# Optimization experiments

Measured on AMD Instinct MI355X. Metric: run time of the kernel, lower is better.

## Reference

```python
import jax, jax.numpy as jnp
import numpy as np
from jax import lax

B, IC, OC, H, W_DIM, K = 8, 64, 64, 256, 512, 3
BLUR_1D = [1.0, 3.0, 3.0, 1.0]
FACTOR = 2
GAIN = 1.0


def _blur_kernel():
    # setup_resample_kernel: outer product of 1D kernel, normalized to sum 1
    k = np.asarray(BLUR_1D, dtype=np.float32)
    k = np.outer(k, k)
    k = k / np.sum(k)
    return k  # [4,4]


def setup_inputs() -> dict:
    key = jax.random.key(0)
    ks = jax.random.split(key, 5)
    x = jax.random.normal(ks[0], (B, IC, H, H), dtype=jnp.float32)
    w = jax.random.normal(ks[1], (B, W_DIM), dtype=jnp.float32)
    # init_std = 1.0 for both weights since lrmul = 1.0
    w_conv = jax.random.normal(ks[2], (K, K, IC, OC), dtype=jnp.float32)
    w_dense = jax.random.normal(ks[3], (W_DIM, IC), dtype=jnp.float32)
    b_mod = jnp.zeros((IC,), dtype=jnp.float32)
    return {"x": x, "w": w, "w_conv": w_conv, "w_dense": w_dense, "b_mod": b_mod}


def reference(x, w, w_conv, w_dense, b_mod):
    k = w_conv.shape[0]
    ic, oc = w_conv.shape[2], w_conv.shape[3]

    # runtime coefs (equalized lr): he_std = gain / sqrt(fan_in), lrmul = 1
    coef_conv = 1.0 / np.sqrt(k * k * ic)
    coef_dense = 1.0 / np.sqrt(w.shape[1])

    # style = Dense(w) + bias (linear act, gain 1) + 1.0   -> [B, IC]
    style = w @ (coef_dense * w_dense) + b_mod + 1.0

    # modulate: [B,k,k,IC,OC]
    wmod = (coef_conv * w_conv)[None] * style[:, None, None, :, None]
    # demodulate over (kh, kw, ic)
    d = lax.rsqrt(jnp.sum(jnp.square(wmod), axis=(1, 2, 3)) + 1e-8)  # [B,OC]
    wmod = wmod * d[:, None, None, None, :]

    # per-sample grouped transposed conv (upsample x2) == lhs-dilated cross-corr
    # with the unflipped modulated weight, padding k-1 on each side.
    w_oihw = jnp.transpose(wmod, (0, 4, 3, 1, 2))  # [B,OC,IC,k,k]

    def up_conv(xb, wb):
        return lax.conv_general_dilated(
            xb[None], wb, window_strides=(1, 1),
            padding=[(k - 1, k - 1), (k - 1, k - 1)],
            lhs_dilation=(FACTOR, FACTOR),
            dimension_numbers=("NCHW", "OIHW", "NCHW"))[0]

    y = jax.vmap(up_conv)(x, w_oihw)  # [B,OC,(H-1)*2+k,(W-1)*2+k] = [B,OC,513,513]

    # upfirdn blur: kernel scaled by gain * factor**2, pad0 = pad1 = 1,
    # true convolution (kernel flipped in reference) applied depthwise.
    kb = jnp.asarray(_blur_kernel() * (GAIN * FACTOR ** 2))  # [4,4]
    fw = kb[::-1, ::-1][None, None]  # [1,1,4,4]
    b_, c_, s1, s2 = y.shape
    y = lax.conv_general_dilated(
        y.reshape(b_ * c_, 1, s1, s2), fw, window_strides=(1, 1),
        padding=[(1, 1), (1, 1)],
        dimension_numbers=("NCHW", "OIHW", "NCHW"))
    # output spatial: s1 + 2 - 4 + 1 = 2H
    return y.reshape(b_, c_, y.shape[2], y.shape[3])
```

## Files before the change

kernel.cpp:

```cpp
#include <hip/hip_runtime.h>

#define NB 8
#define IC 64
#define OC 64
#define HH 256
#define WD 512

typedef __bf16 bf16x8 __attribute__((ext_vector_type(8)));
typedef float f32x16 __attribute__((ext_vector_type(16)));
typedef float f32x2 __attribute__((ext_vector_type(2)));

__global__ __launch_bounds__(64) void style_kernel(
    const float* __restrict__ w, const float* __restrict__ w_dense,
    const float* __restrict__ b_mod, float* __restrict__ style) {
  const int b = blockIdx.x;
  const int ic = threadIdx.x;
  const float coef_dense = 0.044194173824159216f;
  const float* wr = w + b * WD;
  float acc = 0.f;
  for (int k = 0; k < WD; ++k) acc = fmaf(wr[k], w_dense[k * IC + ic], acc);
  style[b * IC + ic] = acc * coef_dense + b_mod[ic] + 1.0f;
}

__device__ inline void compute_E(const float* __restrict__ w_conv,
                                 const float* __restrict__ style, int b, int oc,
                                 int ic, float E[6][6]) {
  const float coef_conv = 1.0f / 24.0f;
  const float s = style[b * IC + ic] * coef_conv;

  float wm[3][3];
  float ssq = 0.f;
  #pragma unroll
  for (int kh = 0; kh < 3; ++kh)
    #pragma unroll
    for (int kw = 0; kw < 3; ++kw) {
      float v = w_conv[((kh * 3 + kw) * IC + ic) * OC + oc] * s;
      wm[kh][kw] = v;
      ssq += v * v;
    }
  #pragma unroll
  for (int off = 32; off > 0; off >>= 1) ssq += __shfl_xor(ssq, off);
  const float d = rsqrtf(ssq + 1e-8f);
  #pragma unroll
  for (int kh = 0; kh < 3; ++kh)
    #pragma unroll
    for (int kw = 0; kw < 3; ++kw) wm[kh][kw] *= d;

  const float g[4] = {0.25f, 0.75f, 0.75f, 0.25f};
  #pragma unroll
  for (int a = 0; a < 6; ++a)
    #pragma unroll
    for (int c = 0; c < 6; ++c) {
      float acc = 0.f;
      #pragma unroll
      for (int dh = 0; dh < 3; ++dh) {
        int u = a - dh;
        if (u < 0 || u > 3) continue;
        #pragma unroll
        for (int dw = 0; dw < 3; ++dw) {
          int v = c - dw;
          if (v < 0 || v > 3) continue;
          acc = fmaf(wm[dh][dw], g[u] * g[v], acc);
        }
      }
      E[a][c] = acc;
    }
}

__global__ __launch_bounds__(64) void pwf_kernel(
    const float* __restrict__ w_conv, const float* __restrict__ style,
    __bf16* __restrict__ PWf) {
  const int oc = blockIdx.x;
  const int b = blockIdx.y;
  const int ic = threadIdx.x;

  float E[6][6];
  compute_E(w_conv, style, b, oc, ic, E);

  const int ks = ic >> 4;
  const int h = (ic >> 3) & 1;
  const int e = ic & 7;
  const int lane = (oc & 31) + 32 * h;
  const int ocg = oc >> 5;

  #pragma unroll
  for (int pp = 0; pp < 2; ++pp)
    #pragma unroll
    for (int pq = 0; pq < 2; ++pq) {
      const int ph = pp * 2 + pq;
      #pragma unroll
      for (int j = 0; j < 3; ++j)
        #pragma unroll
        for (int l = 0; l < 3; ++l) {
          const int tap = j * 3 + l;
          float val = E[2 * j + 1 - pp][2 * l + 1 - pq];
          size_t off =
              ((size_t)(((((b * 4 + ph) * 9 + tap) * 2 + ocg) * 4 + ks)) * 64 +
               lane) * 8 + e;
          PWf[off] = (__bf16)val;
        }
    }
}

__global__ __launch_bounds__(256) void xt_kernel(const float* __restrict__ x,
                                                 __bf16* __restrict__ xT) {
  __shared__ unsigned short buf[64 * 257];
  const int tid = threadIdx.x;
  const int m = blockIdx.x;
  const int b = blockIdx.y;

  for (int ic = 0; ic < 64; ++ic) {
    float v = x[((size_t)(b * 64 + ic) * 256 + m) * 256 + tid];
    __bf16 bv = (__bf16)v;
    buf[ic * 257 + tid] = __builtin_bit_cast(unsigned short, bv);
  }
  __syncthreads();
  bf16x8* xTv = (bf16x8*)xT;
  #pragma unroll
  for (int it = 0; it < 8; ++it) {
    int pix = it * 32 + (tid >> 3);
    int g = tid & 7;
    bf16x8 o;
    #pragma unroll
    for (int e = 0; e < 8; ++e) {
      unsigned short u = buf[(g * 8 + e) * 257 + pix];
      o[e] = __builtin_bit_cast(__bf16, u);
    }
    xTv[((size_t)(b * 256 + m) * 256 + pix) * 8 + g] = o;
  }
}

#define CMT 16
#define CNT 32
#define XR 18
#define XC 34

__device__ __forceinline__ void loadA(const bf16x8* __restrict__ Av, int phb,
                                      int ocg, int ks, int l, int lane,
                                      bf16x8 A[3][2]) {
  #pragma unroll
  for (int j = 0; j < 3; ++j) {
    const int tap = j * 3 + l;
    #pragma unroll
    for (int pq = 0; pq < 2; ++pq)
      A[j][pq] =
          Av[(size_t)((((phb + pq) * 9 + tap) * 2 + ocg) * 4 + ks) * 64 + lane];
  }
}

__global__ __launch_bounds__(512, 2) void conv32_kernel(
    const __bf16* __restrict__ xT, const __bf16* __restrict__ PWf,
    float* __restrict__ out) {
  __shared__ bf16x8 xs[XR * XC * 8];

  const int tid = threadIdx.x;
  const int lane = tid & 63;
  const int w = tid >> 6;
  const int pp = w & 1;
  const int rh = w >> 1;

  const int bx = blockIdx.x;
  const int mtile = bx >> 3;
  const int ntile = bx & 7;
  const int ocg = blockIdx.y;
  const int b = blockIdx.z;
  const int m0 = mtile * CMT;
  const int n0 = ntile * CNT;

  const bf16x8* xTv = (const bf16x8*)xT;
  #pragma unroll
  for (int itr = 0; itr < 10; ++itr) {
    int lin = itr * 512 + tid;
    if (lin < XR * XC * 8) {
      int g = lin & 7;
      int pix = lin >> 3;
      int col = pix % XC;
      int row = pix / XC;
      int gr = m0 - 1 + row;
      int gc = n0 - 1 + col;
      bf16x8 v;
      if ((unsigned)gr < 256u && (unsigned)gc < 256u) {
        v = xTv[((size_t)(b * 256 + gr) * 256 + gc) * 8 + g];
      } else {
        #pragma unroll
        for (int e = 0; e < 8; ++e) v[e] = (__bf16)0.f;
      }
      xs[pix * 8 + (g ^ (col & 7))] = v;
    }
  }
  __syncthreads();

  f32x16 acc[4][2];
  #pragma unroll
  for (int mw = 0; mw < 4; ++mw)
    #pragma unroll
    for (int pq = 0; pq < 2; ++pq)
      #pragma unroll
      for (int e = 0; e < 16; ++e) acc[mw][pq][e] = 0.f;

  const int ln31 = lane & 31;
  const int lh = lane >> 5;
  const bf16x8* Av = (const bf16x8*)PWf;
  const int phb = b * 4 + pp * 2;

  bf16x8 Ac[3][2], An[3][2];
  loadA(Av, phb, ocg, 0, 0, lane, Ac);

  int ks = 0, l = 0;
  #pragma unroll 1
  for (int it = 0; it < 12; ++it) {
    const int ln = (l == 2) ? 0 : l + 1;
    const int ksn = ((l == 2) ? ks + 1 : ks) & 3;
    loadA(Av, phb, ocg, ksn, ln, lane, An);

    bf16x8 Bf[6];
    const int col_t = ln31 + l;
    const int gneed = ks * 2 + lh;
    #pragma unroll
    for (int r = 0; r < 6; ++r) {
      const int lds_row = 4 * rh + r;
      Bf[r] = xs[(lds_row * XC + col_t) * 8 + (gneed ^ (col_t & 7))];
    }

    __builtin_amdgcn_s_setprio(1);
    #pragma unroll
    for (int r = 0; r < 6; ++r) {
      #pragma unroll
      for (int j = 0; j < 3; ++j) {
        const int mw = r - j;
        if (mw >= 0 && mw < 4) {
          acc[mw][0] = __builtin_amdgcn_mfma_f32_32x32x16_bf16(
              Ac[j][0], Bf[r], acc[mw][0], 0, 0, 0);
          acc[mw][1] = __builtin_amdgcn_mfma_f32_32x32x16_bf16(
              Ac[j][1], Bf[r], acc[mw][1], 0, 0, 0);
        }
      }
    }
    __builtin_amdgcn_s_setprio(0);

    #pragma unroll
    for (int j = 0; j < 3; ++j)
      #pragma unroll
      for (int pq = 0; pq < 2; ++pq) Ac[j][pq] = An[j][pq];
    ks = ksn;
    l = ln;
  }

  #pragma unroll
  for (int mw = 0; mw < 4; ++mw) {
    const int p = 2 * (m0 + 4 * rh + mw) + pp;
    #pragma unroll
    for (int rr = 0; rr < 16; ++rr) {
      const int oc_loc = (rr & 3) + 8 * (rr >> 2) + 4 * lh;
      const int oc = ocg * 32 + oc_loc;
      size_t off = ((size_t)(b * 64 + oc) * 512 + p) * 512 + 2 * n0 + 2 * ln31;
      f32x2 v2;
      v2[0] = acc[mw][0][rr];
      v2[1] = acc[mw][1][rr];
      *(f32x2*)(out + off) = v2;
    }
  }
}

__global__ __launch_bounds__(64) void pw_kernel(
    const float* __restrict__ w_conv, const float* __restrict__ style,
    float* __restrict__ PW) {
  const int oc = blockIdx.x;
  const int b = blockIdx.y;
  const int ic = threadIdx.x;
  float E[6][6];
  compute_E(w_conv, style, b, oc, ic, E);
  #pragma unroll
  for (int pp = 0; pp < 2; ++pp)
    #pragma unroll
    for (int pq = 0; pq < 2; ++pq)
      #pragma unroll
      for (int j = 0; j < 3; ++j)
        #pragma unroll
        for (int l = 0; l < 3; ++l)
          PW[(((size_t)((b * 4 + pp * 2 + pq) * OC + oc) * IC + ic) * 9) +
             j * 3 + l] = E[2 * j + 1 - pp][2 * l + 1 - pq];
}

#define MT 16
#define NT 64
#define ICC 8
#define XROWS 18
#define XCOLS 66
#define XSTRIDE 68

__global__ __launch_bounds__(256) void conv_kernel(
    const float* __restrict__ x, const float* __restrict__ PW,
    float* __restrict__ out) {
  __shared__ float lds_x[ICC][XROWS][XSTRIDE];
  __shared__ float lds_w[4][ICC][9][4];

  const int tid = threadIdx.x;
  const int tn = tid & 15;
  const int tm = tid >> 4;
  const int bx = blockIdx.x;
  const int ntile = bx & 3;
  const int mtile = bx >> 2;
  const int ocg = blockIdx.y;
  const int b = blockIdx.z;
  const int m0 = mtile * MT;
  const int n0 = ntile * NT;

  float acc[4][4][4];
  #pragma unroll
  for (int o = 0; o < 4; ++o)
    #pragma unroll
    for (int ph = 0; ph < 4; ++ph)
      #pragma unroll
      for (int s = 0; s < 4; ++s) acc[o][ph][s] = 0.f;

  for (int ic0 = 0; ic0 < IC; ic0 += ICC) {
    __syncthreads();
    for (int ici = 0; ici < ICC; ++ici) {
      const float* xsrc = x + (size_t)(b * IC + ic0 + ici) * HH * HH;
      for (int rc = tid; rc < XROWS * XCOLS; rc += 256) {
        int r = rc / XCOLS;
        int c = rc - r * XCOLS;
        int gr = m0 - 1 + r;
        int gc = n0 - 1 + c;
        float v = 0.f;
        if ((unsigned)gr < HH && (unsigned)gc < HH) v = xsrc[gr * HH + gc];
        lds_x[ici][r][c] = v;
      }
    }
    for (int idx = tid; idx < 4 * ICC * 9 * 4; idx += 256) {
      int o = idx / (ICC * 9 * 4);
      int rem = idx - o * (ICC * 9 * 4);
      int ici = rem / 36;
      int r2 = rem - ici * 36;
      int t = r2 >> 2;
      int ph = r2 & 3;
      lds_w[o][ici][t][ph] =
          PW[(((size_t)((b * 4 + ph) * OC + (ocg * 4 + o)) * IC +
               (ic0 + ici)) * 9) + t];
    }
    __syncthreads();
    for (int ici = 0; ici < ICC; ++ici) {
      #pragma unroll
      for (int j = 0; j < 3; ++j) {
        const float* xr = &lds_x[ici][tm + j][tn * 4];
        float4 a4 = *(const float4*)xr;
        float2 a2 = *(const float2*)(xr + 4);
        float xv[6] = {a4.x, a4.y, a4.z, a4.w, a2.x, a2.y};
        #pragma unroll
        for (int l = 0; l < 3; ++l) {
          #pragma unroll
          for (int o = 0; o < 4; ++o) {
            float4 wv = *(const float4*)&lds_w[o][ici][j * 3 + l][0];
            #pragma unroll
            for (int s = 0; s < 4; ++s) {
              acc[o][0][s] = fmaf(wv.x, xv[l + s], acc[o][0][s]);
              acc[o][1][s] = fmaf(wv.y, xv[l + s], acc[o][1][s]);
              acc[o][2][s] = fmaf(wv.z, xv[l + s], acc[o][2][s]);
              acc[o][3][s] = fmaf(wv.w, xv[l + s], acc[o][3][s]);
            }
          }
        }
      }
    }
  }

  #pragma unroll
  for (int o = 0; o < 4; ++o) {
    #pragma unroll
    for (int pp = 0; pp < 2; ++pp) {
      const int p = 2 * (m0 + tm) + pp;
      float* dst = out +
          (((size_t)(b * OC + ocg * 4 + o) * 512 + p) * 512) + 2 * n0 + 8 * tn;
      float4 v0 = make_float4(acc[o][pp * 2 + 0][0], acc[o][pp * 2 + 1][0],
                              acc[o][pp * 2 + 0][1], acc[o][pp * 2 + 1][1]);
      float4 v1 = make_float4(acc[o][pp * 2 + 0][2], acc[o][pp * 2 + 1][2],
                              acc[o][pp * 2 + 0][3], acc[o][pp * 2 + 1][3]);
      *(float4*)dst = v0;
      *(float4*)(dst + 4) = v1;
    }
  }
}

extern "C" void kernel_launch(void* const* d_in, const int* in_sizes, int n_in,
                              void* d_out, int out_size, void* d_ws,
                              size_t ws_size, hipStream_t stream) {
  const float* x = (const float*)d_in[0];
  const float* w = (const float*)d_in[1];
  const float* w_conv = (const float*)d_in[2];
  const float* w_dense = (const float*)d_in[3];
  const float* b_mod = (const float*)d_in[4];
  float* out = (float*)d_out;

  float* style = (float*)d_ws;

  const size_t PWF_BYTES = (size_t)8 * 4 * 9 * 2 * 4 * 64 * 8 * 2;
  const size_t XT_BYTES = (size_t)8 * 256 * 256 * 64 * 2;
  const size_t NEED = 2048 + PWF_BYTES + XT_BYTES;

  style_kernel<<<NB, 64, 0, stream>>>(w, w_dense, b_mod, style);

  if (ws_size >= NEED) {
    __bf16* PWf = (__bf16*)((char*)d_ws + 2048);
    __bf16* xT = (__bf16*)((char*)d_ws + 2048 + PWF_BYTES);
    pwf_kernel<<<dim3(OC, NB), 64, 0, stream>>>(w_conv, style, PWf);
    xt_kernel<<<dim3(256, NB), 256, 0, stream>>>(x, xT);
    conv32_kernel<<<dim3(128, 2, NB), 512, 0, stream>>>(xT, PWf, out);
  } else {
    float* PW = style + 512;
    pw_kernel<<<dim3(OC, NB), 64, 0, stream>>>(w_conv, style, PW);
    conv_kernel<<<dim3(64, 16, NB), 256, 0, stream>>>(x, PW, out);
  }
}
```

Before: 286.9 us.

## Pre-pad bf16 input, double-buffer LDS tiles via async global-to-LDS loads

Fuses the style computation into the weight-prep kernel, which removes one launch. The transposed bf16 copy of x is now written with a zero halo border, so the conv kernel needs no bounds handling. The conv kernel is restructured so each block processes four column tiles. It double-buffers the input tile in LDS using global_load_lds with an XOR swizzle, overlapping the next tile's load with the current tile's MFMA work. The cost is a larger workspace, more LDS per block, and fewer, longer-lived blocks.

```diff
diff --git a/kernel.cpp b/kernel.cpp
--- a/kernel.cpp
+++ b/kernel.cpp
@@ -5,28 +5,18 @@
 #define OC 64
 #define HH 256
 #define WD 512
+#define PP 258
 
 typedef __bf16 bf16x8 __attribute__((ext_vector_type(8)));
 typedef float f32x16 __attribute__((ext_vector_type(16)));
 typedef float f32x2 __attribute__((ext_vector_type(2)));
-
-__global__ __launch_bounds__(64) void style_kernel(
-    const float* __restrict__ w, const float* __restrict__ w_dense,
-    const float* __restrict__ b_mod, float* __restrict__ style) {
-  const int b = blockIdx.x;
-  const int ic = threadIdx.x;
-  const float coef_dense = 0.044194173824159216f;
-  const float* wr = w + b * WD;
-  float acc = 0.f;
-  for (int k = 0; k < WD; ++k) acc = fmaf(wr[k], w_dense[k * IC + ic], acc);
-  style[b * IC + ic] = acc * coef_dense + b_mod[ic] + 1.0f;
-}
-
-__device__ inline void compute_E(const float* __restrict__ w_conv,
-                                 const float* __restrict__ style, int b, int oc,
-                                 int ic, float E[6][6]) {
+typedef unsigned int u32;
+
+__device__ inline void compute_E(const float* __restrict__ w_conv, float stv,
+                                 int oc, float E[6][6]) {
   const float coef_conv = 1.0f / 24.0f;
-  const float s = style[b * IC + ic] * coef_conv;
+  const float s = stv * coef_conv;
+  const int ic = threadIdx.x & 63;
 
   float wm[3][3];
   float ssq = 0.f;
@@ -67,15 +57,28 @@
     }
 }
 
-__global__ __launch_bounds__(64) void pwf_kernel(
-    const float* __restrict__ w_conv, const float* __restrict__ style,
+__device__ inline float style_of(const float* __restrict__ w,
+                                 const float* __restrict__ w_dense,
+                                 const float* __restrict__ b_mod, int b,
+                                 int ic) {
+  const float coef_dense = 0.044194173824159216f;
+  const float* wr = w + b * WD;
+  float acc = 0.f;
+  for (int k = 0; k < WD; ++k) acc = fmaf(wr[k], w_dense[k * IC + ic], acc);
+  return acc * coef_dense + b_mod[ic] + 1.0f;
+}
+
+__global__ __launch_bounds__(64) void pwfs_kernel(
+    const float* __restrict__ w, const float* __restrict__ w_dense,
+    const float* __restrict__ b_mod, const float* __restrict__ w_conv,
     __bf16* __restrict__ PWf) {
   const int oc = blockIdx.x;
   const int b = blockIdx.y;
   const int ic = threadIdx.x;
 
+  float stv = style_of(w, w_dense, b_mod, b, ic);
   float E[6][6];
-  compute_E(w_conv, style, b, oc, ic, E);
+  compute_E(w_conv, stv, oc, E);
 
   const int ks = ic >> 4;
   const int h = (ic >> 3) & 1;
@@ -102,6 +105,215 @@
     }
 }
 
+__global__ __launch_bounds__(256) void xtp_kernel(const float* __restrict__ x,
+                                                  __bf16* __restrict__ xTg) {
+  __shared__ unsigned short buf[64 * 260];
+  const int tid = threadIdx.x;
+  const int m = blockIdx.x;
+  const int b = blockIdx.y;
+
+  if (m == 256) {
+    uint4 z = make_uint4(0, 0, 0, 0);
+    for (int i = tid; i < 8224; i += 256) {
+      int pix = i >> 3;
+      int sub = i & 7;
+      int pr, pc;
+      if (pix < 258) {
+        pr = 0; pc = pix;
+      } else if (pix < 516) {
+        pr = 257; pc = pix - 258;
+      } else {
+        int rem = pix - 516;
+        pr = 1 + (rem >> 1);
+        pc = (rem & 1) ? 257 : 0;
+      }
+      *(uint4*)(xTg + ((size_t)(b * PP + pr) * PP + pc) * 64 + sub * 8) = z;
+    }
+    return;
+  }
+
+  const int ln = tid & 63, grp = tid >> 6;
+  #pragma unroll
+  for (int p = 0; p < 16; ++p) {
+    const int ic = p * 4 + grp;
+    float4 v = *(const float4*)(x + ((size_t)(b * 64 + ic) * 256 + m) * 256 +
+                                ln * 4);
+    ushort4 u4;
+    u4.x = __builtin_bit_cast(unsigned short, (__bf16)v.x);
+    u4.y = __builtin_bit_cast(unsigned short, (__bf16)v.y);
+    u4.z = __builtin_bit_cast(unsigned short, (__bf16)v.z);
+    u4.w = __builtin_bit_cast(unsigned short, (__bf16)v.w);
+    *(ushort4*)&buf[ic * 260 + ln * 4] = u4;
+  }
+  __syncthreads();
+  #pragma unroll
+  for (int it = 0; it < 8; ++it) {
+    int pix = it * 32 + (tid >> 3);
+    int g = tid & 7;
+    bf16x8 o;
+    #pragma unroll
+    for (int e = 0; e < 8; ++e)
+      o[e] = __builtin_bit_cast(__bf16, buf[(g * 8 + e) * 260 + pix]);
+    *(bf16x8*)(xTg + ((size_t)(b * PP + m + 1) * PP + (pix + 1)) * 64 +
+               g * 8) = o;
+  }
+}
+
+#define CMT 16
+#define CNT 32
+#define XR 18
+#define XC 34
+
+__device__ __forceinline__ void loadA(const bf16x8* __restrict__ Av, int phb,
+                                      int ocg, int ks, int l, int lane,
+                                      bf16x8 A[3][2]) {
+  #pragma unroll
+  for (int j = 0; j < 3; ++j) {
+    const int tap = j * 3 + l;
+    #pragma unroll
+    for (int pq = 0; pq < 2; ++pq)
+      A[j][pq] =
+          Av[(size_t)((((phb + pq) * 9 + tap) * 2 + ocg) * 4 + ks) * 64 + lane];
+  }
+}
+
+#define GLD_LDS(src, dst)                                                \
+  __builtin_amdgcn_global_load_lds(                                      \
+      (const __attribute__((address_space(1))) void*)(src),              \
+      (__attribute__((address_space(3))) void*)(dst), 16, 0, 0)
+
+__device__ __forceinline__ void stage_tile(const __bf16* __restrict__ xTg,
+                                           int b, int m0, int n0,
+                                           __bf16* xsbuf, int wv, int lane) {
+  const int r0 = (18 * wv) >> 3;
+  const int r1 = (18 * (wv + 1)) >> 3;
+  for (int row = r0; row < r1; ++row) {
+    const size_t srow = (size_t)(b * PP + m0 + row) * PP;
+    __bf16* ldsrow = xsbuf + row * (XC * 64);
+    #pragma unroll
+    for (int q = 0; q < 4; ++q) {
+      int pix = q * 8 + (lane >> 3);
+      int g = (lane & 7) ^ (pix & 7);
+      const __bf16* src = xTg + (srow + (n0 + pix)) * 64 + g * 8;
+      GLD_LDS(src, ldsrow + q * 512);
+    }
+    if (lane < 16) {
+      int pix = 32 + (lane >> 3);
+      int g = (lane & 7) ^ (pix & 7);
+      const __bf16* src = xTg + (srow + (n0 + pix)) * 64 + g * 8;
+      GLD_LDS(src, ldsrow + 2048);
+    }
+  }
+}
+
+__global__ __launch_bounds__(512, 2) void conv32p_kernel(
+    const __bf16* __restrict__ xTg, const __bf16* __restrict__ PWf,
+    float* __restrict__ out) {
+  __shared__ __bf16 xs[2][XR * XC * 64];
+
+  const int tid = threadIdx.x;
+  const int lane = tid & 63;
+  const int wv = tid >> 6;
+  const int pp = wv & 1;
+  const int rh = wv >> 1;
+
+  const int bid = blockIdx.x;
+  const int ngrp = bid & 1;
+  const int mtile = (bid >> 1) & 15;
+  const int ocg = (bid >> 5) & 1;
+  const int b = bid >> 6;
+  const int m0 = mtile * CMT;
+
+  const int ln31 = lane & 31;
+  const int lh = lane >> 5;
+  const bf16x8* Av = (const bf16x8*)PWf;
+  const int phb = b * 4 + pp * 2;
+
+  stage_tile(xTg, b, m0, ngrp * 128, &xs[0][0], wv, lane);
+  asm volatile("s_waitcnt vmcnt(0)" ::: "memory");
+  __builtin_amdgcn_s_barrier();
+
+  #pragma unroll 1
+  for (int t = 0; t < 4; ++t) {
+    const int n0 = ngrp * 128 + t * 32;
+    if (t < 3)
+      stage_tile(xTg, b, m0, n0 + 32, &xs[(t + 1) & 1][0], wv, lane);
+
+    const __bf16* xb = &xs[t & 1][0];
+
+    f32x16 acc[4][2];
+    #pragma unroll
+    for (int mw = 0; mw < 4; ++mw)
+      #pragma unroll
+      for (int pq = 0; pq < 2; ++pq)
+        #pragma unroll
+        for (int e = 0; e < 16; ++e) acc[mw][pq][e] = 0.f;
+
+    bf16x8 Ac[3][2], An[3][2];
+    loadA(Av, phb, ocg, 0, 0, lane, Ac);
+
+    int ks = 0, l = 0;
+    #pragma unroll 1
+    for (int it = 0; it < 12; ++it) {
+      const int ln = (l == 2) ? 0 : l + 1;
+      const int ksn = ((l == 2) ? ks + 1 : ks) & 3;
+      loadA(Av, phb, ocg, ksn, ln, lane, An);
+
+      bf16x8 Bf[6];
+      const int col_t = ln31 + l;
+      const int gneed = ks * 2 + lh;
+      #pragma unroll
+      for (int r = 0; r < 6; ++r) {
+        const int lds_row = 4 * rh + r;
+        Bf[r] = *(const bf16x8*)(xb + ((lds_row * XC + col_t) * 8 +
+                                       (gneed ^ (col_t & 7))) * 8);
+      }
+
+      __builtin_amdgcn_s_setprio(1);
+      #pragma unroll
+      for (int r = 0; r < 6; ++r) {
+        #pragma unroll
+        for (int j = 0; j < 3; ++j) {
+          const int mw = r - j;
+          if (mw >= 0 && mw < 4) {
+            acc[mw][0] = __builtin_amdgcn_mfma_f32_32x32x16_bf16(
+                Ac[j][0], Bf[r], acc[mw][0], 0, 0, 0);
+            acc[mw][1] = __builtin_amdgcn_mfma_f32_32x32x16_bf16(
+                Ac[j][1], Bf[r], acc[mw][1], 0, 0, 0);
+          }
+        }
+      }
+      __builtin_amdgcn_s_setprio(0);
+
+      #pragma unroll
+      for (int j = 0; j < 3; ++j)
+        #pragma unroll
+        for (int pq = 0; pq < 2; ++pq) Ac[j][pq] = An[j][pq];
+      ks = ksn;
+      l = ln;
+    }
+
+    #pragma unroll
+    for (int mw = 0; mw < 4; ++mw) {
+      const int p = 2 * (m0 + 4 * rh + mw) + pp;
+      #pragma unroll
+      for (int rr = 0; rr < 16; ++rr) {
+        const int oc_loc = (rr & 3) + 8 * (rr >> 2) + 4 * lh;
+        const int oc = ocg * 32 + oc_loc;
+        size_t off =
+            ((size_t)(b * 64 + oc) * 512 + p) * 512 + 2 * n0 + 2 * ln31;
+        f32x2 v2;
+        v2[0] = acc[mw][0][rr];
+        v2[1] = acc[mw][1][rr];
+        *(f32x2*)(out + off) = v2;
+      }
+    }
+
+    asm volatile("s_waitcnt vmcnt(63)" ::: "memory");
+    __builtin_amdgcn_s_barrier();
+  }
+}
+
 __global__ __launch_bounds__(256) void xt_kernel(const float* __restrict__ x,
                                                  __bf16* __restrict__ xT) {
   __shared__ unsigned short buf[64 * 257];
@@ -111,8 +323,7 @@
 
   for (int ic = 0; ic < 64; ++ic) {
     float v = x[((size_t)(b * 64 + ic) * 256 + m) * 256 + tid];
-    __bf16 bv = (__bf16)v;
-    buf[ic * 257 + tid] = __builtin_bit_cast(unsigned short, bv);
+    buf[ic * 257 + tid] = __builtin_bit_cast(unsigned short, (__bf16)v);
   }
   __syncthreads();
   bf16x8* xTv = (bf16x8*)xT;
@@ -122,29 +333,9 @@
     int g = tid & 7;
     bf16x8 o;
     #pragma unroll
-    for (int e = 0; e < 8; ++e) {
-      unsigned short u = buf[(g * 8 + e) * 257 + pix];
-      o[e] = __builtin_bit_cast(__bf16, u);
-    }
+    for (int e = 0; e < 8; ++e)
+      o[e] = __builtin_bit_cast(__bf16, buf[(g * 8 + e) * 257 + pix]);
     xTv[((size_t)(b * 256 + m) * 256 + pix) * 8 + g] = o;
-  }
-}
-
-#define CMT 16
-#define CNT 32
-#define XR 18
-#define XC 34
-
-__device__ __forceinline__ void loadA(const bf16x8* __restrict__ Av, int phb,
-                                      int ocg, int ks, int l, int lane,
-                                      bf16x8 A[3][2]) {
-  #pragma unroll
-  for (int j = 0; j < 3; ++j) {
-    const int tap = j * 3 + l;
-    #pragma unroll
-    for (int pq = 0; pq < 2; ++pq)
-      A[j][pq] =
-          Av[(size_t)((((phb + pq) * 9 + tap) * 2 + ocg) * 4 + ks) * 64 + lane];
   }
 }
 
@@ -263,13 +454,15 @@
 }
 
 __global__ __launch_bounds__(64) void pw_kernel(
-    const float* __restrict__ w_conv, const float* __restrict__ style,
+    const float* __restrict__ w, const float* __restrict__ w_dense,
+    const float* __restrict__ b_mod, const float* __restrict__ w_conv,
     float* __restrict__ PW) {
   const int oc = blockIdx.x;
   const int b = blockIdx.y;
   const int ic = threadIdx.x;
+  float stv = style_of(w, w_dense, b_mod, b, ic);
   float E[6][6];
-  compute_E(w_conv, style, b, oc, ic, E);
+  compute_E(w_conv, stv, oc, E);
   #pragma unroll
   for (int pp = 0; pp < 2; ++pp)
     #pragma unroll
@@ -392,23 +585,29 @@
   const float* b_mod = (const float*)d_in[4];
   float* out = (float*)d_out;
 
-  float* style = (float*)d_ws;
-
   const size_t PWF_BYTES = (size_t)8 * 4 * 9 * 2 * 4 * 64 * 8 * 2;
+  const size_t XTG_BYTES = (size_t)8 * PP * PP * 64 * 2;
   const size_t XT_BYTES = (size_t)8 * 256 * 256 * 64 * 2;
-  const size_t NEED = 2048 + PWF_BYTES + XT_BYTES;
-
-  style_kernel<<<NB, 64, 0, stream>>>(w, w_dense, b_mod, style);
-
-  if (ws_size >= NEED) {
-    __bf16* PWf = (__bf16*)((char*)d_ws + 2048);
-    __bf16* xT = (__bf16*)((char*)d_ws + 2048 + PWF_BYTES);
-    pwf_kernel<<<dim3(OC, NB), 64, 0, stream>>>(w_conv, style, PWf);
+  const size_t NEED_NEW = PWF_BYTES + XTG_BYTES;
+  const size_t NEED_OLD = PWF_BYTES + XT_BYTES;
+
+  if (ws_size >= NEED_NEW) {
+    __bf16* PWf = (__bf16*)d_ws;
+    __bf16* xTg = (__bf16*)((char*)d_ws + PWF_BYTES);
+    pwfs_kernel<<<dim3(OC, NB), 64, 0, stream>>>(w, w_dense, b_mod, w_conv,
+                                                 PWf);
+    xtp_kernel<<<dim3(257, NB), 256, 0, stream>>>(x, xTg);
+    conv32p_kernel<<<dim3(512), 512, 0, stream>>>(xTg, PWf, out);
+  } else if (ws_size >= NEED_OLD) {
+    __bf16* PWf = (__bf16*)d_ws;
+    __bf16* xT = (__bf16*)((char*)d_ws + PWF_BYTES);
+    pwfs_kernel<<<dim3(OC, NB), 64, 0, stream>>>(w, w_dense, b_mod, w_conv,
+                                                 PWf);
     xt_kernel<<<dim3(256, NB), 256, 0, stream>>>(x, xT);
     conv32_kernel<<<dim3(128, 2, NB), 512, 0, stream>>>(xT, PWf, out);
   } else {
-    float* PW = style + 512;
-    pw_kernel<<<dim3(OC, NB), 64, 0, stream>>>(w_conv, style, PW);
+    float* PW = (float*)d_ws;
+    pw_kernel<<<dim3(OC, NB), 64, 0, stream>>>(w, w_dense, b_mod, w_conv, PW);
     conv_kernel<<<dim3(64, 16, NB), 256, 0, stream>>>(x, PW, out);
   }
 }
```

After: 285.1 us. About the same (-0.6%).
